# Kernel optimization log

Measured on AMD Instinct MI355X. Metric: run time of the kernel, lower is better.

The kernel has to match this reference:

```python
import jax, jax.numpy as jnp
import numpy as np

B, S, D = 2, 2048, 512
WIN = 64  # local causal window (includes current token)
EPS = 1e-5


def setup_inputs() -> dict:
    key = jax.random.key(0)
    ks = jax.random.split(key, 8)
    sc = 0.02
    return {
        "x":  jax.random.normal(ks[0], (B, S, D), jnp.float32),
        "Wq": jax.random.normal(ks[1], (D, D), jnp.float32) * sc,
        "bq": jnp.zeros((D,), jnp.float32),
        "Wk": jax.random.normal(ks[2], (D, D), jnp.float32) * sc,
        "bk": jnp.zeros((D,), jnp.float32),
        "Wv": jax.random.normal(ks[3], (D, D), jnp.float32) * sc,
        "bv": jnp.zeros((D,), jnp.float32),
        "Wo": jax.random.normal(ks[4], (D, D), jnp.float32) * sc,
        "bo": jnp.zeros((D,), jnp.float32),
        "Wr": jax.random.normal(ks[5], (D, D), jnp.float32) * sc,
        "br": jnp.zeros((D,), jnp.float32),
        "gamma": jnp.ones((D,), jnp.float32),
        "beta":  jnp.zeros((D,), jnp.float32),
    }


def _layernorm(h, gamma, beta):
    mu = jnp.mean(h, axis=-1, keepdims=True)
    var = jnp.mean(jnp.square(h - mu), axis=-1, keepdims=True)
    return (h - mu) * jax.lax.rsqrt(var + EPS) * gamma + beta


def _local_attention(x, Wq, bq, Wk, bk, Wv, bv, Wo, bo):
    q = x @ Wq + bq
    k = x @ Wk + bk
    v = x @ Wv + bv
    kp = jnp.pad(k, ((0, 0), (WIN - 1, 0), (0, 0)))
    vp = jnp.pad(v, ((0, 0), (WIN - 1, 0), (0, 0)))
    idx = jnp.arange(S)[:, None] + jnp.arange(WIN)[None, :]
    kw = kp[:, idx, :]
    vw = vp[:, idx, :]
    scores = jnp.einsum('bsd,bswd->bsw', q, kw) / np.float32(np.sqrt(D))
    valid = (idx >= (WIN - 1 - jnp.zeros((), jnp.int32)))  # padded slots invalid
    valid = idx >= (WIN - 1) - jnp.arange(S)[:, None] * 0
    valid = (idx - (WIN - 1)) >= 0  # key position in original seq >= 0
    scores = jnp.where(valid[None, :, :], scores, jnp.float32(-1e9))
    attn = jax.nn.softmax(scores, axis=-1)
    out = jnp.einsum('bsw,bswd->bsd', attn, vw)
    return out @ Wo + bo


def reference(x, Wq, bq, Wk, bk, Wv, bv, Wo, bo, Wr, br, gamma, beta):
    read = _local_attention(x, Wq, bq, Wk, bk, Wv, bv, Wo, bo)
    sence = x @ Wr + br
    read = _layernorm(read, gamma, beta)
    sence = _layernorm(sence, gamma, beta)
    return jax.nn.gelu(read + sence, approximate=False)
```

## Files before the change

### kernel.cpp

```cpp
#include <hip/hip_runtime.h>
#include <hip/hip_bf16.h>
#include <math.h>

#define BB 2
#define SS 2048
#define DD 512
#define MTOT 4096

typedef __attribute__((ext_vector_type(8))) short sv8;
typedef __attribute__((ext_vector_type(4))) float f32x4;

static const size_t OFF_XB   = 0;
static const size_t OFF_WT   = 4194304;
static const size_t OFF_BIAS = 6815744;
static const size_t OFF_Y    = 6823936;
static const size_t OFF_VT   = 19406848;
static const size_t OFF_READ = 23601152;
static const size_t OFF_PP   = 27795456;
static const size_t OFF_ATT  = 0;

static __device__ __forceinline__ float bf2f(short s) {
    unsigned u = ((unsigned)(unsigned short)s) << 16;
    return __builtin_bit_cast(float, u);
}
static __device__ __forceinline__ short f2bf(float f) {
    unsigned u = __builtin_bit_cast(unsigned, f);
    unsigned r = 0x7fffu + ((u >> 16) & 1u);
    u += r;
    return (short)(u >> 16);
}

#define GLOAD_LDS16(gp, lp)                                                        \
    __builtin_amdgcn_global_load_lds(                                              \
        (const __attribute__((address_space(1))) unsigned*)(gp),                   \
        (__attribute__((address_space(3))) unsigned*)(lp), 16, 0, 0)

__global__ __launch_bounds__(256) void prep_all(const float* __restrict__ x,
                                                const float* __restrict__ Wq,
                                                const float* __restrict__ Wk,
                                                const float* __restrict__ Wv,
                                                const float* __restrict__ Wr,
                                                const float* __restrict__ Wo,
                                                const float* __restrict__ bq,
                                                const float* __restrict__ bk,
                                                const float* __restrict__ bv,
                                                const float* __restrict__ br,
                                                short* __restrict__ xb,
                                                short* __restrict__ wt,
                                                float* __restrict__ ball) {
    int z = blockIdx.z;
    int tid = threadIdx.x;
    if (z == 5) {
        int flat = blockIdx.y * 16 + blockIdx.x;
        if (flat == 0) {
#pragma unroll
            for (int it = 0; it < 8; ++it) {
                int i = it * 256 + tid;
                int sel = i >> 9;
                const float* src = (sel == 0) ? bq : (sel == 1) ? bk : (sel == 2) ? bv : br;
                ball[i] = src[i & 511];
            }
        }
        for (int i = flat * 256 + tid; i < MTOT * DD / 4; i += 256 * 256) {
            float4 v = ((const float4*)x)[i];
            short4 o;
            o.x = f2bf(v.x); o.y = f2bf(v.y); o.z = f2bf(v.z); o.w = f2bf(v.w);
            ((short4*)xb)[i] = o;
        }
        return;
    }
    __shared__ float tile[32][33];
    const float* W = (z == 0) ? Wq : (z == 1) ? Wk : (z == 2) ? Wv : (z == 3) ? Wr : Wo;
    int k0 = blockIdx.y * 32, n0 = blockIdx.x * 32;
    int tx = tid & 31, ty = tid >> 5;
    for (int r = ty; r < 32; r += 8)
        tile[r][tx] = W[(size_t)(k0 + r) * 512 + n0 + tx];
    __syncthreads();
    short* o = wt + (size_t)z * 512 * 512;
    for (int r = ty; r < 32; r += 8)
        o[(size_t)(n0 + r) * 512 + k0 + tx] = f2bf(tile[tx][r]);
}

template <int GEMM1>
__global__ __launch_bounds__(256) void gemm_bt(const short* __restrict__ A,
                                               const short* __restrict__ Bt,
                                               const float* __restrict__ bias,
                                               short* __restrict__ Cout, int ldc,
                                               short* __restrict__ vt) {
    __shared__ __align__(16) short lbuf[2 * 128 * 64];
    short* lA = lbuf;
    short* lB = lbuf + 128 * 64;
    int tid = threadIdx.x;
    int mbase = blockIdx.y * 128;
    int nbase = blockIdx.x * 128;
    int lane = tid & 63, wave = tid >> 6;
    int wm = wave >> 1, wn = wave & 1;
    bool vswap = GEMM1 && (nbase >= 1024) && (nbase < 1536);

    f32x4 acc[4][4] = {};

    int srow = (lane >> 3);
    int scol = (lane & 7) * 8;

    for (int k0 = 0; k0 < 512; k0 += 64) {
#pragma unroll
        for (int c = 0; c < 4; ++c) {
            int ch = wave * 4 + c;
            int row = ch * 8 + srow;
            GLOAD_LDS16(A + (size_t)(mbase + row) * 512 + k0 + scol, &lA[ch * 512]);
            GLOAD_LDS16(Bt + (size_t)(nbase + row) * 512 + k0 + scol, &lB[ch * 512]);
        }
        __syncthreads();
#pragma unroll
        for (int kk = 0; kk < 2; ++kk) {
            int koff = kk * 32 + (lane >> 4) * 8;
            sv8 af[4], bfr[4];
#pragma unroll
            for (int m = 0; m < 4; ++m)
                af[m] = *(const sv8*)&lA[(wm * 64 + m * 16 + (lane & 15)) * 64 + koff];
#pragma unroll
            for (int n = 0; n < 4; ++n)
                bfr[n] = *(const sv8*)&lB[(wn * 64 + n * 16 + (lane & 15)) * 64 + koff];
            if (!vswap) {
#pragma unroll
                for (int m = 0; m < 4; ++m)
#pragma unroll
                    for (int n = 0; n < 4; ++n)
                        acc[m][n] = __builtin_amdgcn_mfma_f32_16x16x32_bf16(
                            af[m], bfr[n], acc[m][n], 0, 0, 0);
            } else {
#pragma unroll
                for (int m = 0; m < 4; ++m)
#pragma unroll
                    for (int n = 0; n < 4; ++n)
                        acc[m][n] = __builtin_amdgcn_mfma_f32_16x16x32_bf16(
                            bfr[n], af[m], acc[m][n], 0, 0, 0);
            }
        }
        __syncthreads();
    }

    int r0 = (lane >> 4) * 4, c0 = lane & 15;
    if (!vswap) {
        short* sC = lbuf;
#pragma unroll
        for (int m = 0; m < 4; ++m)
#pragma unroll
            for (int n = 0; n < 4; ++n) {
                int cl = wn * 64 + n * 16 + c0;
                float bv = bias[nbase + cl];
#pragma unroll
                for (int j = 0; j < 4; ++j) {
                    int rl = wm * 64 + m * 16 + r0 + j;
                    sC[rl * 128 + cl] = f2bf(acc[m][n][j] + bv);
                }
            }
        __syncthreads();
        int nybase = (GEMM1 && nbase >= 1536) ? nbase - 512 : nbase;
#pragma unroll
        for (int it = 0; it < 8; ++it) {
            int idx = it * 256 + tid;
            int row = idx >> 4, slot = idx & 15;
            sv8 v = *(const sv8*)&sC[row * 128 + slot * 8];
            *(sv8*)&Cout[(size_t)(mbase + row) * ldc + nybase + slot * 8] = v;
        }
    } else {
        int bb = mbase >> 11, tb = mbase & 2047;
#pragma unroll
        for (int m = 0; m < 4; ++m)
#pragma unroll
            for (int n = 0; n < 4; ++n) {
                int dglob = nbase + wn * 64 + n * 16 + r0;
                int d = dglob - 1024;
                int tl = tb + wm * 64 + m * 16 + c0;
#pragma unroll
                for (int j = 0; j < 4; ++j) {
                    float v = acc[m][n][j] + bias[dglob + j];
                    vt[((size_t)bb * 512 + d + j) * 2048 + tl] = f2bf(v);
                }
            }
    }
}

__global__ __launch_bounds__(256) void attn_scores(const short* __restrict__ Y,
                                                   short* __restrict__ Pp) {
    __shared__ float sS[64][132];
    int tile = blockIdx.x;
    int b = tile >> 5;
    int t0 = (tile & 31) * 64;
    int s0 = tile * 64;
    int tid = threadIdx.x, lane = tid & 63, wave = tid >> 6;
    int wm = wave >> 1, wn = wave & 1;

    f32x4 acc[2][4] = {};
    const short* Q = Y;
    const short* Kb = Y + 512;

    int arow[2], brow[4];
#pragma unroll
    for (int m = 0; m < 2; ++m) arow[m] = s0 + wm * 32 + m * 16 + (lane & 15);
#pragma unroll
    for (int n = 0; n < 4; ++n) {
        int kr = t0 - 64 + wn * 64 + n * 16 + (lane & 15);
        if (kr < 0) kr = 0;
        brow[n] = (b << 11) + kr;
    }
#pragma unroll
    for (int step = 0; step < 16; ++step) {
        int koff = step * 32 + (lane >> 4) * 8;
        sv8 af[2], bfr[4];
#pragma unroll
        for (int m = 0; m < 2; ++m)
            af[m] = *(const sv8*)(Q + (size_t)arow[m] * 1536 + koff);
#pragma unroll
        for (int n = 0; n < 4; ++n)
            bfr[n] = *(const sv8*)(Kb + (size_t)brow[n] * 1536 + koff);
#pragma unroll
        for (int m = 0; m < 2; ++m)
#pragma unroll
            for (int n = 0; n < 4; ++n)
                acc[m][n] = __builtin_amdgcn_mfma_f32_16x16x32_bf16(
                    af[m], bfr[n], acc[m][n], 0, 0, 0);
    }
    int r0 = (lane >> 4) * 4, c0 = lane & 15;
#pragma unroll
    for (int m = 0; m < 2; ++m)
#pragma unroll
        for (int n = 0; n < 4; ++n) {
            int jc = wn * 64 + n * 16 + c0;
#pragma unroll
            for (int j = 0; j < 4; ++j)
                sS[wm * 32 + m * 16 + r0 + j][jc] =
                    acc[m][n][j] * 0.04419417382415922f;
        }
    __syncthreads();

    int q = tid >> 2, j0 = (tid & 3) * 32;
    float v[32];
    float mx = -1e30f;
    int jlo = q + 1;
    int jmin0 = 64 - t0;
    if (jmin0 > jlo) jlo = jmin0;
    int jhi = q + 64;
#pragma unroll
    for (int jj = 0; jj < 32; ++jj) {
        int j = j0 + jj;
        bool ok = (j >= jlo) && (j <= jhi);
        float s = ok ? sS[q][j] : -1e30f;
        v[jj] = s;
        mx = fmaxf(mx, s);
    }
    mx = fmaxf(mx, __shfl_xor(mx, 1));
    mx = fmaxf(mx, __shfl_xor(mx, 2));
    float sum = 0.f;
#pragma unroll
    for (int jj = 0; jj < 32; ++jj) {
        float e = (v[jj] > -1e29f) ? __expf(v[jj] - mx) : 0.f;
        v[jj] = e;
        sum += e;
    }
    sum += __shfl_xor(sum, 1);
    sum += __shfl_xor(sum, 2);
    float inv = 1.f / sum;
    short* dst = Pp + (size_t)tile * 8192 + q * 128 + j0;
#pragma unroll
    for (int k = 0; k < 4; ++k) {
        sv8 o;
#pragma unroll
        for (int e = 0; e < 8; ++e) o[e] = f2bf(v[k * 8 + e] * inv);
        *(sv8*)(dst + k * 8) = o;
    }
}

__global__ __launch_bounds__(256) void attn_pv(const short* __restrict__ Pp,
                                               const short* __restrict__ Vt,
                                               short* __restrict__ att) {
    int tile = blockIdx.y, dchunk = blockIdx.x;
    int b = tile >> 5;
    int t0 = (tile & 31) * 64;
    int s0 = tile * 64;
    int tid = threadIdx.x, lane = tid & 63, wave = tid >> 6;
    int wm = wave >> 1, wn = wave & 1;

    f32x4 acc[2][4] = {};
    const short* Pbase = Pp + (size_t)tile * 8192;
#pragma unroll
    for (int ks = 0; ks < 4; ++ks) {
        int koff = ks * 32 + (lane >> 4) * 8;
        sv8 af[2], bfr[4];
#pragma unroll
        for (int m = 0; m < 2; ++m)
            af[m] = *(const sv8*)(Pbase + (wm * 32 + m * 16 + (lane & 15)) * 128 + koff);
#pragma unroll
        for (int n = 0; n < 4; ++n) {
            int d = dchunk * 128 + wn * 64 + n * 16 + (lane & 15);
            long off = (long)(b * 512 + d) * 2048 + (t0 - 64 + koff);
            bfr[n] = *(const sv8*)(Vt + off);
        }
#pragma unroll
        for (int m = 0; m < 2; ++m)
#pragma unroll
            for (int n = 0; n < 4; ++n)
                acc[m][n] = __builtin_amdgcn_mfma_f32_16x16x32_bf16(
                    af[m], bfr[n], acc[m][n], 0, 0, 0);
    }
    int r0 = (lane >> 4) * 4, c0 = lane & 15;
#pragma unroll
    for (int m = 0; m < 2; ++m)
#pragma unroll
        for (int n = 0; n < 4; ++n) {
            int col = dchunk * 128 + wn * 64 + n * 16 + c0;
#pragma unroll
            for (int j = 0; j < 4; ++j) {
                int row = s0 + wm * 32 + m * 16 + r0 + j;
                att[(size_t)row * 512 + col] = f2bf(acc[m][n][j]);
            }
        }
}

__global__ __launch_bounds__(256) void ln_gelu(const short* __restrict__ readb,
                                               const short* __restrict__ Y,
                                               const float* __restrict__ gamma,
                                               const float* __restrict__ beta,
                                               float* __restrict__ out) {
    int row = blockIdx.x * 4 + (threadIdx.x >> 6);
    int lane = threadIdx.x & 63;
    sv8 rv = *(const sv8*)(readb + (size_t)row * 512 + lane * 8);
    sv8 sv = *(const sv8*)(Y + (size_t)row * 1536 + 1024 + lane * 8);
    float rf[8], sf[8];
    float sr = 0.f, sr2 = 0.f, ss = 0.f, ss2 = 0.f;
#pragma unroll
    for (int e = 0; e < 8; ++e) {
        rf[e] = bf2f(rv[e]); sf[e] = bf2f(sv[e]);
        sr += rf[e]; sr2 += rf[e] * rf[e];
        ss += sf[e]; ss2 += sf[e] * sf[e];
    }
#pragma unroll
    for (int off = 32; off; off >>= 1) {
        sr += __shfl_xor(sr, off);
        sr2 += __shfl_xor(sr2, off);
        ss += __shfl_xor(ss, off);
        ss2 += __shfl_xor(ss2, off);
    }
    float mu_r = sr * (1.f / 512.f);
    float is_r = rsqrtf(sr2 * (1.f / 512.f) - mu_r * mu_r + 1e-5f);
    float mu_s = ss * (1.f / 512.f);
    float is_s = rsqrtf(ss2 * (1.f / 512.f) - mu_s * mu_s + 1e-5f);

    float4 ga = ((const float4*)gamma)[lane * 2];
    float4 gb = ((const float4*)gamma)[lane * 2 + 1];
    float4 ba = ((const float4*)beta)[lane * 2];
    float4 bb = ((const float4*)beta)[lane * 2 + 1];
    float g[8] = {ga.x, ga.y, ga.z, ga.w, gb.x, gb.y, gb.z, gb.w};
    float be[8] = {ba.x, ba.y, ba.z, ba.w, bb.x, bb.y, bb.z, bb.w};

    float y[8];
#pragma unroll
    for (int e = 0; e < 8; ++e) {
        float xv = (rf[e] - mu_r) * is_r * g[e] + be[e] +
                   (sf[e] - mu_s) * is_s * g[e] + be[e];
        y[e] = 0.5f * xv * (1.f + erff(xv * 0.70710678118654752f));
    }
    float* o = out + (size_t)row * 512 + lane * 8;
    ((float4*)o)[0] = make_float4(y[0], y[1], y[2], y[3]);
    ((float4*)o)[1] = make_float4(y[4], y[5], y[6], y[7]);
}

extern "C" void kernel_launch(void* const* d_in, const int* in_sizes, int n_in,
                              void* d_out, int out_size, void* d_ws, size_t ws_size,
                              hipStream_t stream) {
    const float* x  = (const float*)d_in[0];
    const float* Wq = (const float*)d_in[1];
    const float* bq = (const float*)d_in[2];
    const float* Wk = (const float*)d_in[3];
    const float* bk = (const float*)d_in[4];
    const float* Wv = (const float*)d_in[5];
    const float* bv = (const float*)d_in[6];
    const float* Wo = (const float*)d_in[7];
    const float* bo = (const float*)d_in[8];
    const float* Wr = (const float*)d_in[9];
    const float* br = (const float*)d_in[10];
    const float* gamma = (const float*)d_in[11];
    const float* beta  = (const float*)d_in[12];

    char* ws = (char*)d_ws;
    short* xb    = (short*)(ws + OFF_XB);
    short* wt    = (short*)(ws + OFF_WT);
    float* ball  = (float*)(ws + OFF_BIAS);
    short* Y     = (short*)(ws + OFF_Y);
    short* vtb   = (short*)(ws + OFF_VT);
    short* readb = (short*)(ws + OFF_READ);
    short* Pp    = (short*)(ws + OFF_PP);
    short* att   = (short*)(ws + OFF_ATT);

    prep_all<<<dim3(16, 16, 6), 256, 0, stream>>>(x, Wq, Wk, Wv, Wr, Wo,
                                                  bq, bk, bv, br, xb, wt, ball);

    gemm_bt<1><<<dim3(16, 32), 256, 0, stream>>>(xb, wt, ball, Y, 1536, vtb);

    attn_scores<<<64, 256, 0, stream>>>(Y, Pp);
    attn_pv<<<dim3(4, 64), 256, 0, stream>>>(Pp, vtb, att);

    gemm_bt<0><<<dim3(4, 32), 256, 0, stream>>>(att, wt + (size_t)4 * 512 * 512, bo,
                                                readb, 512, nullptr);

    ln_gelu<<<1024, 256, 0, stream>>>(readb, Y, gamma, beta, (float*)d_out);
}
```

Measured before the change: 154.3 us.

## Fold output projection Wo into value projection weights and bias

Precomputes Wv·Wo (and bv·Wo + bo) on device before the main QKV GEMM, so the attention PV output directly yields the projected result. This removes the separate M=4096 output-projection GEMM, trading it for a small 512×512×512 GEMM and a serial bias dot product in the prep kernel. Adds one extra bf16 rounding of the fused weight matrix.

```diff
diff --git a/kernel.cpp b/kernel.cpp
--- a/kernel.cpp
+++ b/kernel.cpp
@@ -10,14 +10,14 @@
 typedef __attribute__((ext_vector_type(8))) short sv8;
 typedef __attribute__((ext_vector_type(4))) float f32x4;
 
-static const size_t OFF_XB   = 0;
-static const size_t OFF_WT   = 4194304;
-static const size_t OFF_BIAS = 6815744;
-static const size_t OFF_Y    = 6823936;
-static const size_t OFF_VT   = 19406848;
-static const size_t OFF_READ = 23601152;
-static const size_t OFF_PP   = 27795456;
-static const size_t OFF_ATT  = 0;
+static const size_t OFF_XB    = 0;
+static const size_t OFF_WT    = 4194304;
+static const size_t OFF_BIAS  = 6815744;
+static const size_t OFF_Y     = 6823936;
+static const size_t OFF_VT    = 19406848;
+static const size_t OFF_READ  = 23601152;
+static const size_t OFF_PP    = 27795456;
+static const size_t OFF_WVRAW = 28844032;
 
 static __device__ __forceinline__ float bf2f(short s) {
     unsigned u = ((unsigned)(unsigned short)s) << 16;
@@ -45,8 +45,10 @@
                                                 const float* __restrict__ bk,
                                                 const float* __restrict__ bv,
                                                 const float* __restrict__ br,
+                                                const float* __restrict__ bo,
                                                 short* __restrict__ xb,
                                                 short* __restrict__ wt,
+                                                short* __restrict__ wvraw,
                                                 float* __restrict__ ball) {
     int z = blockIdx.z;
     int tid = threadIdx.x;
@@ -57,8 +59,16 @@
             for (int it = 0; it < 8; ++it) {
                 int i = it * 256 + tid;
                 int sel = i >> 9;
-                const float* src = (sel == 0) ? bq : (sel == 1) ? bk : (sel == 2) ? bv : br;
-                ball[i] = src[i & 511];
+                if (sel == 2) {
+                    int c = i - 1024;
+                    float acc = bo[c];
+                    for (int j = 0; j < 512; ++j)
+                        acc += bv[j] * Wo[(size_t)j * 512 + c];
+                    ball[i] = acc;
+                } else {
+                    const float* src = (sel == 0) ? bq : (sel == 1) ? bk : br;
+                    ball[i] = src[i & 511];
+                }
             }
         }
         for (int i = flat * 256 + tid; i < MTOT * DD / 4; i += 256 * 256) {
@@ -73,8 +83,11 @@
     const float* W = (z == 0) ? Wq : (z == 1) ? Wk : (z == 2) ? Wv : (z == 3) ? Wr : Wo;
     int k0 = blockIdx.y * 32, n0 = blockIdx.x * 32;
     int tx = tid & 31, ty = tid >> 5;
-    for (int r = ty; r < 32; r += 8)
-        tile[r][tx] = W[(size_t)(k0 + r) * 512 + n0 + tx];
+    for (int r = ty; r < 32; r += 8) {
+        float val = W[(size_t)(k0 + r) * 512 + n0 + tx];
+        tile[r][tx] = val;
+        if (z == 2) wvraw[(size_t)(k0 + r) * 512 + n0 + tx] = f2bf(val);
+    }
     __syncthreads();
     short* o = wt + (size_t)z * 512 * 512;
     for (int r = ty; r < 32; r += 8)
@@ -95,7 +108,7 @@
     int nbase = blockIdx.x * 128;
     int lane = tid & 63, wave = tid >> 6;
     int wm = wave >> 1, wn = wave & 1;
-    bool vswap = GEMM1 && (nbase >= 1024) && (nbase < 1536);
+    bool vswap = (GEMM1 == 1) && (nbase >= 1024) && (nbase < 1536);
 
     f32x4 acc[4][4] = {};
 
@@ -148,7 +161,7 @@
 #pragma unroll
             for (int n = 0; n < 4; ++n) {
                 int cl = wn * 64 + n * 16 + c0;
-                float bv = bias[nbase + cl];
+                float bv = (GEMM1 == 2) ? 0.f : bias[nbase + cl];
 #pragma unroll
                 for (int j = 0; j < 4; ++j) {
                     int rl = wm * 64 + m * 16 + r0 + j;
@@ -156,7 +169,7 @@
                 }
             }
         __syncthreads();
-        int nybase = (GEMM1 && nbase >= 1536) ? nbase - 512 : nbase;
+        int nybase = (GEMM1 == 1 && nbase >= 1536) ? nbase - 512 : nbase;
 #pragma unroll
         for (int it = 0; it < 8; ++it) {
             int idx = it * 256 + tid;
@@ -274,7 +287,7 @@
 
 __global__ __launch_bounds__(256) void attn_pv(const short* __restrict__ Pp,
                                                const short* __restrict__ Vt,
-                                               short* __restrict__ att) {
+                                               short* __restrict__ readb) {
     int tile = blockIdx.y, dchunk = blockIdx.x;
     int b = tile >> 5;
     int t0 = (tile & 31) * 64;
@@ -313,7 +326,7 @@
 #pragma unroll
             for (int j = 0; j < 4; ++j) {
                 int row = s0 + wm * 32 + m * 16 + r0 + j;
-                att[(size_t)row * 512 + col] = f2bf(acc[m][n][j]);
+                readb[(size_t)row * 512 + col] = f2bf(acc[m][n][j]);
             }
         }
 }
@@ -391,18 +404,19 @@
     short* vtb   = (short*)(ws + OFF_VT);
     short* readb = (short*)(ws + OFF_READ);
     short* Pp    = (short*)(ws + OFF_PP);
-    short* att   = (short*)(ws + OFF_ATT);
+    short* wvraw = (short*)(ws + OFF_WVRAW);
 
     prep_all<<<dim3(16, 16, 6), 256, 0, stream>>>(x, Wq, Wk, Wv, Wr, Wo,
-                                                  bq, bk, bv, br, xb, wt, ball);
+                                                  bq, bk, bv, br, bo, xb, wt, wvraw, ball);
+
+    gemm_bt<2><<<dim3(4, 4), 256, 0, stream>>>(wt + (size_t)4 * 512 * 512, wvraw,
+                                               nullptr, wt + (size_t)2 * 512 * 512,
+                                               512, nullptr);
 
     gemm_bt<1><<<dim3(16, 32), 256, 0, stream>>>(xb, wt, ball, Y, 1536, vtb);
 
     attn_scores<<<64, 256, 0, stream>>>(Y, Pp);
-    attn_pv<<<dim3(4, 64), 256, 0, stream>>>(Pp, vtb, att);
-
-    gemm_bt<0><<<dim3(4, 32), 256, 0, stream>>>(att, wt + (size_t)4 * 512 * 512, bo,
-                                                readb, 512, nullptr);
+    attn_pv<<<dim3(4, 64), 256, 0, stream>>>(Pp, vtb, readb);
 
     ln_gelu<<<1024, 256, 0, stream>>>(readb, Y, gamma, beta, (float*)d_out);
 }
```

Measured after the change: 181.6 us. 17.7% more time.
